# Kernel optimization log

Hardware: AMD Instinct MI355X
Metric: run time of the kernel (lower is better)

The kernel has to match this reference:

```python
import jax, jax.numpy as jnp
import numpy as np

IN_FEATURES = 4096
OUT_FEATURES = 11008
NUM_GROUPS = 4


def setup_inputs() -> dict:
    key = jax.random.key(0)
    k1, k2, k3 = jax.random.split(key, 3)
    inp = jax.random.normal(k1, (16, IN_FEATURES), dtype=jnp.float32)
    # packed int2 weights: each byte holds 4 ternary values (stored biased by +1 in 2 bits)
    weight_packed = jax.random.randint(k2, (OUT_FEATURES, IN_FEATURES // 4), 0, 256, dtype=jnp.int32)
    weight_scale = jax.random.uniform(k3, (NUM_GROUPS,), dtype=jnp.float32, minval=0.5, maxval=1.5)
    return {"input": inp, "weight_packed": weight_packed, "weight_scale": weight_scale}


def _unpack_int2(weight_packed):
    # [M, K/4] packed bytes -> [M, K] ternary values in {-1, 0, 1, 2}
    p = weight_packed
    M, Kp = p.shape
    w = jnp.stack([p & 3, (p >> 2) & 3, (p >> 4) & 3, (p >> 6) & 3], axis=-1)
    return w.reshape(M, Kp * 4).astype(jnp.float32) - 1.0


def reference(input, weight_packed, weight_scale):
    # per-row int8 activation quantization
    s = 127.0 / jnp.clip(jnp.max(jnp.abs(input), axis=-1, keepdims=True), 1e-5)  # [B,1]
    q = jnp.clip(jnp.round(input * s), -128.0, 127.0)  # int8-valued floats [B,K]
    w = _unpack_int2(weight_packed)  # [M,K]
    out = q @ w.T  # [B,M] integer-valued accumulation
    M = weight_packed.shape[0]
    rows_per_group = M // weight_scale.shape[0]
    col_scale = jnp.repeat(weight_scale, rows_per_group)  # [M] per-output-group scale
    return out * (1.0 / s) * col_scale
```

## Files before the change

kernel.cpp:

```cpp
#include <hip/hip_runtime.h>
#include <stdint.h>

#define K_DIM 4096
#define KW 1024
#define M_DIM 11008
#define B_DIM 16
#define GROUP_ROWS 2752

typedef int v4i __attribute__((ext_vector_type(4)));

__device__ __forceinline__ int spread2(int p) {
    int t = p | (p << 12);
    return (t & 0x00030003) | (((t >> 2) & 0x00030003) << 8);
}

__global__ __launch_bounds__(1024) void quant_k(const float* __restrict__ in,
                                                int* __restrict__ qg,
                                                int* __restrict__ sumq,
                                                float* __restrict__ invs) {
    const int b = blockIdx.x, t = threadIdx.x;
    const int lane = t & 63, wid = t >> 6;

    float4 v = ((const float4*)(in + (size_t)b * K_DIM))[t];
    float mx = fmaxf(fmaxf(fabsf(v.x), fabsf(v.y)), fmaxf(fabsf(v.z), fabsf(v.w)));
#pragma unroll
    for (int s = 1; s < 64; s <<= 1) mx = fmaxf(mx, __shfl_xor(mx, s, 64));

    __shared__ float wmax[16];
    __shared__ int wsum[16];
    if (lane == 0) wmax[wid] = mx;
    __syncthreads();
    float bm = wmax[0];
#pragma unroll
    for (int i = 1; i < 16; ++i) bm = fmaxf(bm, wmax[i]);
    const float sc = 127.f / fmaxf(bm, 1e-5f);

    float xs[4] = {v.x, v.y, v.z, v.w};
    int w = 0, ss = 0;
#pragma unroll
    for (int j = 0; j < 4; ++j) {
        int q = (int)rintf(xs[j] * sc);
        q = q > 127 ? 127 : (q < -128 ? -128 : q);
        ss += q;
        w |= (q & 255) << (8 * j);
    }
    qg[b * KW + t] = w;

#pragma unroll
    for (int s = 1; s < 64; s <<= 1) ss += __shfl_xor(ss, s, 64);
    if (lane == 0) wsum[wid] = ss;
    __syncthreads();
    if (t == 0) {
        int tot = 0;
#pragma unroll
        for (int i = 0; i < 16; ++i) tot += wsum[i];
        sumq[b] = tot;
        invs[b] = fmaxf(bm, 1e-5f) / 127.f;
    }
}

__global__ __launch_bounds__(256) void gemm_k(const int* __restrict__ wp,
                                              const int* __restrict__ qg,
                                              const int* __restrict__ sumq,
                                              const float* __restrict__ invs,
                                              const float* __restrict__ wscale,
                                              float* __restrict__ out) {
    __shared__ int red[4][64][4];
    const int t = threadIdx.x, lane = t & 63, wid = t >> 6;
    const int m0 = blockIdx.x * 16;
    const int lrow = lane & 15;
    const int lgrp = lane >> 4;
    const int wbase = wid * 256 + lgrp * 4;

    const int* wptr = wp + (size_t)(m0 + lrow) * KW + wbase;
    const int* qptr = qg + lrow * KW + wbase;

    v4i qv0 = *(const v4i*)qptr;
    v4i wv[16];
#pragma unroll
    for (int s = 0; s < 16; ++s) wv[s] = *(const v4i*)(wptr + s * 16);

    v4i acc = {0, 0, 0, 0};
    v4i qA = qv0, qB;
#pragma unroll
    for (int s = 0; s < 16; ++s) {
        if (s < 15) {
            if ((s & 1) == 0) qB = *(const v4i*)(qptr + (s + 1) * 16);
            else              qA = *(const v4i*)(qptr + (s + 1) * 16);
        }
        v4i bb;
        bb[0] = spread2(wv[s][0]); bb[1] = spread2(wv[s][1]);
        bb[2] = spread2(wv[s][2]); bb[3] = spread2(wv[s][3]);
        v4i aa = ((s & 1) == 0) ? qA : qB;
        acc = __builtin_amdgcn_mfma_i32_16x16x64_i8(aa, bb, acc, 0, 0, 0);
    }

    *((v4i*)&red[wid][lane][0]) = acc;
    __syncthreads();

    const int b = t >> 4, m = t & 15;
    const int src_lane = ((b >> 2) << 4) | m;
    const int reg = b & 3;
    int sum = red[0][src_lane][reg] + red[1][src_lane][reg] +
              red[2][src_lane][reg] + red[3][src_lane][reg];
    const float gscale = wscale[m0 / GROUP_ROWS];
    const float val = (float)(sum - sumq[b]) * invs[b] * gscale;
    out[(size_t)b * M_DIM + m0 + m] = val;
}

extern "C" void kernel_launch(void* const* d_in, const int* in_sizes, int n_in,
                              void* d_out, int out_size, void* d_ws, size_t ws_size,
                              hipStream_t stream) {
    const float* inp    = (const float*)d_in[0];
    const int*   wp     = (const int*)d_in[1];
    const float* wscale = (const float*)d_in[2];
    float* out = (float*)d_out;

    int*   qg   = (int*)d_ws;
    int*   sumq = qg + B_DIM * KW;
    float* invs = (float*)(sumq + B_DIM);

    quant_k<<<dim3(B_DIM), dim3(1024), 0, stream>>>(inp, qg, sumq, invs);
    gemm_k<<<dim3(M_DIM / 16), dim3(256), 0, stream>>>(wp, qg, sumq, invs, wscale, out);
}
```

Baseline: 22.52 us.

## Stage weight tiles through double-buffered LDS with coalesced row loads

Weights are now loaded so that each wavefront reads a contiguous 1 KB slice of a row, which gives fully coalesced global reads instead of the earlier per-lane strided 16-byte pieces. The slices are written into a double-buffered, XOR-swizzled LDS tile and read back in MFMA operand layout. The K dimension is processed in four quarters, with the next quarter's loads issued before the current one is computed. In exchange the kernel adds LDS traffic and several barriers per block, and it holds fewer weights in registers at once.

Result: faster. 21.24 us (-5.7%).

```diff
diff --git a/kernel.cpp b/kernel.cpp
--- a/kernel.cpp
+++ b/kernel.cpp
@@ -6,6 +6,7 @@
 #define M_DIM 11008
 #define B_DIM 16
 #define GROUP_ROWS 2752
+#define QTR_W 256
 
 typedef int v4i __attribute__((ext_vector_type(4)));
 
@@ -65,46 +66,77 @@
                                               const float* __restrict__ invs,
                                               const float* __restrict__ wscale,
                                               float* __restrict__ out) {
-    __shared__ int red[4][64][4];
+    __shared__ v4i buf[2][1024];
     const int t = threadIdx.x, lane = t & 63, wid = t >> 6;
     const int m0 = blockIdx.x * 16;
     const int lrow = lane & 15;
     const int lgrp = lane >> 4;
-    const int wbase = wid * 256 + lgrp * 4;
 
-    const int* wptr = wp + (size_t)(m0 + lrow) * KW + wbase;
-    const int* qptr = qg + lrow * KW + wbase;
-
-    v4i qv0 = *(const v4i*)qptr;
-    v4i wv[16];
-#pragma unroll
-    for (int s = 0; s < 16; ++s) wv[s] = *(const v4i*)(wptr + s * 16);
+    const int* qbase = qg + lrow * KW + wid * 64 + lgrp * 4;
 
     v4i acc = {0, 0, 0, 0};
-    v4i qA = qv0, qB;
+    v4i wst[4];
+    v4i qb[2][4];
+
 #pragma unroll
-    for (int s = 0; s < 16; ++s) {
-        if (s < 15) {
-            if ((s & 1) == 0) qB = *(const v4i*)(qptr + (s + 1) * 16);
-            else              qA = *(const v4i*)(qptr + (s + 1) * 16);
+    for (int r = 0; r < 4; ++r) {
+        const int row = r * 4 + wid;
+        wst[r] = *(const v4i*)(wp + (size_t)(m0 + row) * KW + lane * 4);
+    }
+#pragma unroll
+    for (int s = 0; s < 4; ++s) qb[0][s] = *(const v4i*)(qbase + s * 16);
+#pragma unroll
+    for (int r = 0; r < 4; ++r) {
+        const int row = r * 4 + wid;
+        buf[0][row * 64 + (lane ^ (row & 7))] = wst[r];
+    }
+    asm volatile("s_waitcnt lgkmcnt(0)" ::: "memory");
+    asm volatile("s_barrier" ::: "memory");
+
+#pragma unroll
+    for (int q = 0; q < 4; ++q) {
+        if (q < 3) {
+#pragma unroll
+            for (int r = 0; r < 4; ++r) {
+                const int row = r * 4 + wid;
+                wst[r] = *(const v4i*)(wp + (size_t)(m0 + row) * KW + (q + 1) * QTR_W + lane * 4);
+            }
+#pragma unroll
+            for (int s = 0; s < 4; ++s)
+                qb[(q + 1) & 1][s] = *(const v4i*)(qbase + (q + 1) * QTR_W + s * 16);
         }
-        v4i bb;
-        bb[0] = spread2(wv[s][0]); bb[1] = spread2(wv[s][1]);
-        bb[2] = spread2(wv[s][2]); bb[3] = spread2(wv[s][3]);
-        v4i aa = ((s & 1) == 0) ? qA : qB;
-        acc = __builtin_amdgcn_mfma_i32_16x16x64_i8(aa, bb, acc, 0, 0, 0);
+#pragma unroll
+        for (int s = 0; s < 4; ++s) {
+            const int c = wid * 16 + s * 4 + lgrp;
+            v4i wv = buf[q & 1][lrow * 64 + (c ^ (lrow & 7))];
+            v4i bb;
+            bb[0] = spread2(wv[0]); bb[1] = spread2(wv[1]);
+            bb[2] = spread2(wv[2]); bb[3] = spread2(wv[3]);
+            acc = __builtin_amdgcn_mfma_i32_16x16x64_i8(qb[q & 1][s], bb, acc, 0, 0, 0);
+        }
+        asm volatile("s_barrier" ::: "memory");
+        if (q < 3) {
+#pragma unroll
+            for (int r = 0; r < 4; ++r) {
+                const int row = r * 4 + wid;
+                buf[(q + 1) & 1][row * 64 + (lane ^ (row & 7))] = wst[r];
+            }
+            asm volatile("s_waitcnt lgkmcnt(0)" ::: "memory");
+            asm volatile("s_barrier" ::: "memory");
+        }
     }
 
-    *((v4i*)&red[wid][lane][0]) = acc;
-    __syncthreads();
+    buf[0][wid * 64 + lane] = acc;
+    asm volatile("s_waitcnt lgkmcnt(0)" ::: "memory");
+    asm volatile("s_barrier" ::: "memory");
 
     const int b = t >> 4, m = t & 15;
     const int src_lane = ((b >> 2) << 4) | m;
     const int reg = b & 3;
-    int sum = red[0][src_lane][reg] + red[1][src_lane][reg] +
-              red[2][src_lane][reg] + red[3][src_lane][reg];
-    const float gscale = wscale[m0 / GROUP_ROWS];
-    const float val = (float)(sum - sumq[b]) * invs[b] * gscale;
+    const int* red = (const int*)&buf[0][0];
+    int sum = red[(0 * 64 + src_lane) * 4 + reg] + red[(1 * 64 + src_lane) * 4 + reg] +
+              red[(2 * 64 + src_lane) * 4 + reg] + red[(3 * 64 + src_lane) * 4 + reg];
+    const float val = (float)(sum - sumq[b]) * invs[b] * wscale[m0 / GROUP_ROWS];
     out[(size_t)b * M_DIM + m0 + m] = val;
 }
 
```

## Coalesce weight loads via swizzled LDS staging with nontemporal loads

Applied to the files above, without the earlier changes.

Weight rows are now loaded so that 16 consecutive lanes read contiguous 64-byte spans of one row, using nontemporal loads, rather than each lane striding across rows. The data is then written to a XOR-swizzled shared buffer and read back in the MFMA operand layout. All activation fragments are preloaded into registers, and launch bounds request 2 blocks per CU. This aims to improve global coalescing of the dominant weight stream, at the cost of 64KB of LDS per block plus extra LDS traffic and register pressure.

Result: faster. 19.94 us (-11.4%).

```diff
diff --git a/kernel.cpp b/kernel.cpp
--- a/kernel.cpp
+++ b/kernel.cpp
@@ -59,52 +59,62 @@
     }
 }
 
-__global__ __launch_bounds__(256) void gemm_k(const int* __restrict__ wp,
-                                              const int* __restrict__ qg,
-                                              const int* __restrict__ sumq,
-                                              const float* __restrict__ invs,
-                                              const float* __restrict__ wscale,
-                                              float* __restrict__ out) {
-    __shared__ int red[4][64][4];
+__global__ __launch_bounds__(256, 2) void gemm_k(const int* __restrict__ wp,
+                                                 const int* __restrict__ qg,
+                                                 const int* __restrict__ sumq,
+                                                 const float* __restrict__ invs,
+                                                 const float* __restrict__ wscale,
+                                                 float* __restrict__ out) {
+    __shared__ v4i wbuf[4 * 1024];
+    __shared__ int red[4 * 64 * 4];
     const int t = threadIdx.x, lane = t & 63, wid = t >> 6;
     const int m0 = blockIdx.x * 16;
     const int lrow = lane & 15;
     const int lgrp = lane >> 4;
-    const int wbase = wid * 256 + lgrp * 4;
 
-    const int* wptr = wp + (size_t)(m0 + lrow) * KW + wbase;
-    const int* qptr = qg + lrow * KW + wbase;
+    v4i qr[16];
+#pragma unroll
+    for (int s = 0; s < 16; ++s)
+        qr[s] = *(const v4i*)(qg + lrow * KW + wid * 256 + s * 16 + lgrp * 4);
 
-    v4i qv0 = *(const v4i*)qptr;
-    v4i wv[16];
+    v4i wst[16];
 #pragma unroll
-    for (int s = 0; s < 16; ++s) wv[s] = *(const v4i*)(wptr + s * 16);
+    for (int c = 0; c < 4; ++c)
+#pragma unroll
+        for (int i = 0; i < 4; ++i) {
+            const int row = i * 4 + lgrp;
+            wst[c * 4 + i] = __builtin_nontemporal_load(
+                (const v4i*)(wp + (size_t)(m0 + row) * KW + wid * 256 + c * 64 + lrow * 4));
+        }
 
     v4i acc = {0, 0, 0, 0};
-    v4i qA = qv0, qB;
 #pragma unroll
-    for (int s = 0; s < 16; ++s) {
-        if (s < 15) {
-            if ((s & 1) == 0) qB = *(const v4i*)(qptr + (s + 1) * 16);
-            else              qA = *(const v4i*)(qptr + (s + 1) * 16);
+    for (int c = 0; c < 4; ++c) {
+#pragma unroll
+        for (int i = 0; i < 4; ++i) {
+            const int row = i * 4 + lgrp;
+            wbuf[wid * 1024 + c * 256 + row * 16 + (lrow ^ (row & 7))] = wst[c * 4 + i];
         }
-        v4i bb;
-        bb[0] = spread2(wv[s][0]); bb[1] = spread2(wv[s][1]);
-        bb[2] = spread2(wv[s][2]); bb[3] = spread2(wv[s][3]);
-        v4i aa = ((s & 1) == 0) ? qA : qB;
-        acc = __builtin_amdgcn_mfma_i32_16x16x64_i8(aa, bb, acc, 0, 0, 0);
+        asm volatile("s_waitcnt lgkmcnt(0)" ::: "memory");
+#pragma unroll
+        for (int sp = 0; sp < 4; ++sp) {
+            v4i wv = wbuf[wid * 1024 + c * 256 + lrow * 16 + ((sp * 4 + lgrp) ^ (lrow & 7))];
+            v4i bb;
+            bb[0] = spread2(wv[0]); bb[1] = spread2(wv[1]);
+            bb[2] = spread2(wv[2]); bb[3] = spread2(wv[3]);
+            acc = __builtin_amdgcn_mfma_i32_16x16x64_i8(qr[c * 4 + sp], bb, acc, 0, 0, 0);
+        }
     }
 
-    *((v4i*)&red[wid][lane][0]) = acc;
+    *(v4i*)(red + (wid * 64 + lane) * 4) = acc;
     __syncthreads();
 
     const int b = t >> 4, m = t & 15;
     const int src_lane = ((b >> 2) << 4) | m;
     const int reg = b & 3;
-    int sum = red[0][src_lane][reg] + red[1][src_lane][reg] +
-              red[2][src_lane][reg] + red[3][src_lane][reg];
-    const float gscale = wscale[m0 / GROUP_ROWS];
-    const float val = (float)(sum - sumq[b]) * invs[b] * gscale;
+    int sum = red[(0 * 64 + src_lane) * 4 + reg] + red[(1 * 64 + src_lane) * 4 + reg] +
+              red[(2 * 64 + src_lane) * 4 + reg] + red[(3 * 64 + src_lane) * 4 + reg];
+    const float val = (float)(sum - sumq[b]) * invs[b] * wscale[m0 / GROUP_ROWS];
     out[(size_t)b * M_DIM + m0 + m] = val;
 }
 
```
